# Performance work log

Measured on AMD Instinct MI355X. Metric: run time of the kernel, lower is better.

## Reference

```python
import jax, jax.numpy as jnp
import numpy as np

E = 768   # embedding_dim
D = 64    # head_dim
B = 8
S = 2048


def setup_inputs() -> dict:
    key = jax.random.key(0)
    k1, k2, k3, k4 = jax.random.split(key, 4)
    inputs = jax.random.normal(k1, (B, S, E), dtype=jnp.float32)
    # causal mask: 1 where attending allowed, 0 elsewhere (masked_fill where ==0)
    attention_mask = jnp.tril(jnp.ones((S, S), dtype=jnp.int32))[None, :, :]
    Q = jax.random.normal(k2, (E, D), dtype=jnp.float32) * 0.01
    K = jax.random.normal(k3, (E, D), dtype=jnp.float32) * 0.01
    V = jax.random.normal(k4, (E, D), dtype=jnp.float32) * 0.01
    return {"inputs": inputs, "attention_mask": attention_mask, "Q": Q, "K": K, "V": V}


def reference(inputs, attention_mask, Q, K, V):
    scale = 1.0 / np.sqrt(D).astype(np.float32)
    q = inputs @ Q          # [B,S,D]
    k = inputs @ K          # [B,S,D]
    v = inputs @ V          # [B,S,D]
    w = jnp.einsum('bqd,bkd->bqk', q, k) * scale   # [B,S,S]
    w = jnp.where(attention_mask == 0, -jnp.inf, w)
    attn = jax.nn.softmax(w, axis=-1)              # [B,S,S]
    states = attn @ v                              # [B,S,D] (dropout p=0.0 is identity)
    return states
```

## Files before the change

### kernel.cpp

```cpp
#include <hip/hip_runtime.h>
#include <cstdint>

#define B_ 8
#define S_ 2048
#define E_ 768
#define D_ 64
#define NSPLIT 4
#define SEGLEN (S_ / NSPLIT)
#define ROWS (B_ * S_)

typedef unsigned short ushort_t;
typedef __attribute__((ext_vector_type(8))) short s16x8;
typedef __attribute__((ext_vector_type(4))) float f32x4;

__device__ inline ushort_t f2bf(float f) {
  unsigned int x = __float_as_uint(f);
  return (ushort_t)((x + 0x7fffu + ((x >> 16) & 1u)) >> 16);
}

__device__ inline unsigned int pkbf(float hi, float lo) {
  return __builtin_amdgcn_perm(__float_as_uint(hi) + 0x8000u,
                               __float_as_uint(lo) + 0x8000u, 0x07060302u);
}

__device__ inline void async16(const void* g, void* l) {
  __builtin_amdgcn_global_load_lds(
      (const __attribute__((address_space(1))) unsigned int*)g,
      (__attribute__((address_space(3))) unsigned int*)l, 16, 0, 0);
}

__global__ __launch_bounds__(256) void wt_kernel(
    const float* __restrict__ Wq, const float* __restrict__ Wk,
    const float* __restrict__ Wv, ushort_t* __restrict__ wt) {
  const int mat = blockIdx.y;
  const int e = blockIdx.x * 4 + (threadIdx.x >> 6);
  const int d = threadIdx.x & 63;
  const float* W = (mat == 0) ? Wq : ((mat == 1) ? Wk : Wv);
  wt[(long)(mat * 64 + d) * E_ + e] = f2bf(W[(long)e * D_ + d]);
}

__global__ __launch_bounds__(256) void qkv_mfma(
    const float* __restrict__ in, const ushort_t* __restrict__ wt,
    ushort_t* __restrict__ qb, ushort_t* __restrict__ kb,
    ushort_t* __restrict__ vtb) {
  const int tid = threadIdx.x;
  const int w = tid >> 6;
  const int L = tid & 63;
  const int c = L & 15;
  const int q = L >> 4;
  const int row0 = blockIdx.x * 32;

  __shared__ float Alds[2][32][64];
  __shared__ ushort_t Blds[2][192][64];

  const int ar0 = w * 8 + (L >> 4);
  const int ar1 = ar0 + 4;
  const int asl = L & 15;
  const float* asrc0 = in + (long)(row0 + ar0) * E_ + ((asl ^ (ar0 & 15)) << 2);
  const float* asrc1 = in + (long)(row0 + ar1) * E_ + ((asl ^ (ar1 & 15)) << 2);
  const int bsl = L & 7;
  const ushort_t* bsrc[6];
#pragma unroll
  for (int jj = 0; jj < 6; ++jj) {
    const int br = w * 48 + jj * 8 + (L >> 3);
    bsrc[jj] = wt + (long)br * E_ + ((bsl ^ (br & 7)) << 3);
  }
  float* ad[2] = {&Alds[0][w * 8][0], &Alds[1][w * 8][0]};
  ushort_t* bd[2] = {&Blds[0][w * 48][0], &Blds[1][w * 48][0]};

  const int mloc = w & 1;
  const int nbase = (w >> 1) * 6;
  const int ra = mloc * 16 + c;
  const int offA00 = ra * 256 + ((2 * q + 0) ^ c) * 16;
  const int offA01 = ra * 256 + ((2 * q + 1) ^ c) * 16;
  const int offA10 = ra * 256 + ((8 + 2 * q + 0) ^ c) * 16;
  const int offA11 = ra * 256 + ((8 + 2 * q + 1) ^ c) * 16;
  int offB0[6], offB1[6];
#pragma unroll
  for (int t = 0; t < 6; ++t) {
    const int n = (nbase + t) * 16 + c;
    offB0[t] = n * 128 + ((q + 0) ^ (c & 7)) * 16;
    offB1[t] = n * 128 + ((q + 4) ^ (c & 7)) * 16;
  }
  const char* Abase = (const char*)&Alds[0][0][0];
  const char* Bbase = (const char*)&Blds[0][0][0];

  f32x4 acc[6];
#pragma unroll
  for (int n = 0; n < 6; ++n) acc[n] = (f32x4){0.f, 0.f, 0.f, 0.f};

  async16(asrc0, ad[0]);
  async16(asrc1, ad[0] + 4 * 64);
#pragma unroll
  for (int jj = 0; jj < 6; ++jj) async16(bsrc[jj], bd[0] + jj * 8 * 64);
  asrc0 += 64; asrc1 += 64;
#pragma unroll
  for (int jj = 0; jj < 6; ++jj) bsrc[jj] += 64;

  for (int it = 0; it < E_ / 64; ++it) {
    const int b = it & 1;
    __syncthreads();
    if (it + 1 < E_ / 64) {
      const int nb = 1 - b;
      async16(asrc0, ad[nb]);
      async16(asrc1, ad[nb] + 4 * 64);
#pragma unroll
      for (int jj = 0; jj < 6; ++jj) async16(bsrc[jj], bd[nb] + jj * 8 * 64);
      asrc0 += 64; asrc1 += 64;
#pragma unroll
      for (int jj = 0; jj < 6; ++jj) bsrc[jj] += 64;
    }
    const char* Ab = Abase + b * 8192;
    const char* Bb = Bbase + b * 24576;
    const float4 a00 = *(const float4*)(Ab + offA00);
    const float4 a01 = *(const float4*)(Ab + offA01);
    const float4 a10 = *(const float4*)(Ab + offA10);
    const float4 a11 = *(const float4*)(Ab + offA11);
    union { s16x8 v; unsigned int u[4]; } af0, af1;
    af0.u[0] = pkbf(a00.y, a00.x);
    af0.u[1] = pkbf(a00.w, a00.z);
    af0.u[2] = pkbf(a01.y, a01.x);
    af0.u[3] = pkbf(a01.w, a01.z);
    af1.u[0] = pkbf(a10.y, a10.x);
    af1.u[1] = pkbf(a10.w, a10.z);
    af1.u[2] = pkbf(a11.y, a11.x);
    af1.u[3] = pkbf(a11.w, a11.z);
#pragma unroll
    for (int t = 0; t < 6; ++t) {
      const s16x8 bf0 = *(const s16x8*)(Bb + offB0[t]);
      const s16x8 bf1 = *(const s16x8*)(Bb + offB1[t]);
      acc[t] = __builtin_amdgcn_mfma_f32_16x16x32_bf16(af0.v, bf0, acc[t], 0, 0, 0);
      acc[t] = __builtin_amdgcn_mfma_f32_16x16x32_bf16(af1.v, bf1, acc[t], 0, 0, 0);
    }
  }

  const float qscale = 0.125f * 1.44269504088896340736f;
  const int row0w = row0 + mloc * 16;
  const int b_ = row0w >> 11;
  const int srow = row0w & (S_ - 1);
#pragma unroll
  for (int n = 0; n < 6; ++n) {
    const int gn = nbase + n;
    const int mat = gn >> 2;
    const int d0 = (gn & 3) * 16 + c;
#pragma unroll
    for (int reg = 0; reg < 4; ++reg) {
      const int m = q * 4 + reg;
      const float x = acc[n][reg];
      if (mat == 0) {
        qb[(long)(row0w + m) * D_ + d0] = f2bf(x * qscale);
      } else if (mat == 1) {
        kb[(long)(row0w + m) * D_ + d0] = f2bf(x);
      } else {
        vtb[(long)b_ * D_ * S_ + (long)d0 * S_ + srow + m] = f2bf(x);
      }
    }
  }
}

__global__ __launch_bounds__(256) void attn_mfma(
    const ushort_t* __restrict__ qb, const ushort_t* __restrict__ kb,
    const ushort_t* __restrict__ vtb, float* __restrict__ op,
    float* __restrict__ lw) {
  const int qb0 = blockIdx.x * 64;
  const int batch = blockIdx.y;
  const int seg = blockIdx.z;
  const int j0 = seg * SEGLEN;
  const int jmax = min(j0 + SEGLEN, qb0 + 64);
  if (j0 >= jmax) return;
  const int ntiles = (jmax - j0) >> 6;

  const int w = threadIdx.x >> 6;
  const int L = threadIdx.x & 63;
  const int col = L & 15;
  const int quad = L >> 4;

  __shared__ ushort_t Kl[2][64][64];
  __shared__ ushort_t Vl[2][64][64];
  __shared__ ushort_t Pl[4][16][72];

  const ushort_t* kbb = kb + (long)batch * S_ * D_;
  const ushort_t* vbb = vtb + (long)batch * D_ * S_;

  const int rl = (w << 4) + (L >> 3);
  const int gsw = (L & 7) ^ (rl & 7);
  const ushort_t* ksrc = kbb + ((long)(j0 + rl) << 6) + gsw * 8;
  const ushort_t* vsrc = vbb + (long)rl * S_ + j0 + gsw * 8;
  ushort_t* kdst[2] = {&Kl[0][w * 16][0], &Kl[1][w * 16][0]};
  ushort_t* vdst[2] = {&Vl[0][w * 16][0], &Vl[1][w * 16][0]};

  const int s0 = ((quad ^ (col & 7)) * 16);

  const ushort_t* qrow = qb + ((long)(batch * S_ + qb0 + w * 16 + col) * D_);
  const s16x8 qf0 = *(const s16x8*)(qrow + quad * 8);
  const s16x8 qf1 = *(const s16x8*)(qrow + 32 + quad * 8);

  f32x4 O[4];
#pragma unroll
  for (int t = 0; t < 4; ++t) O[t] = (f32x4){0.f, 0.f, 0.f, 0.f};
  float l[4] = {0.f, 0.f, 0.f, 0.f};

  async16(ksrc, kdst[0]);
  async16(ksrc + 512, kdst[0] + 512);
  async16(vsrc, vdst[0]);
  async16(vsrc + 8 * S_, vdst[0] + 512);
  ksrc += 64 * 64; vsrc += 64;

  for (int i = 0; i < ntiles; ++i) {
    const int b = i & 1;
    const int kt = j0 + i * 64;
    __syncthreads();
    if (i + 1 < ntiles) {
      const int nb = 1 - b;
      async16(ksrc, kdst[nb]);
      async16(ksrc + 512, kdst[nb] + 512);
      async16(vsrc, vdst[nb]);
      async16(vsrc + 8 * S_, vdst[nb] + 512);
      ksrc += 64 * 64; vsrc += 64;
    }
    const char* Kb = (const char*)&Kl[b][0][0];
    const char* Vb = (const char*)&Vl[b][0][0];

    f32x4 S[4];
#pragma unroll
    for (int t = 0; t < 4; ++t) {
      const s16x8 kf0 = *(const s16x8*)(Kb + (t * 16 + col) * 128 + s0);
      const s16x8 kf1 = *(const s16x8*)(Kb + (t * 16 + col) * 128 + (s0 ^ 64));
      f32x4 z = (f32x4){0.f, 0.f, 0.f, 0.f};
      z = __builtin_amdgcn_mfma_f32_16x16x32_bf16(qf0, kf0, z, 0, 0, 0);
      S[t] = __builtin_amdgcn_mfma_f32_16x16x32_bf16(qf1, kf1, z, 0, 0, 0);
    }
    if (kt + 64 > qb0) {
#pragma unroll
      for (int t = 0; t < 4; ++t) {
        const int colg = kt + t * 16 + col;
#pragma unroll
        for (int reg = 0; reg < 4; ++reg) {
          const int rowg = qb0 + w * 16 + quad * 4 + reg;
          if (colg > rowg) S[t][reg] = -1e30f;
        }
      }
    }
    float P[4][4];
#pragma unroll
    for (int t = 0; t < 4; ++t)
#pragma unroll
      for (int reg = 0; reg < 4; ++reg) {
        P[t][reg] = exp2f(S[t][reg]);
        l[reg] += P[t][reg];
      }
#pragma unroll
    for (int t = 0; t < 4; ++t)
#pragma unroll
      for (int reg = 0; reg < 4; ++reg)
        Pl[w][quad * 4 + reg][t * 16 + col] = f2bf(P[t][reg]);
    const s16x8 p0 = *(const s16x8*)&Pl[w][col][quad * 8];
    const s16x8 p1 = *(const s16x8*)&Pl[w][col][32 + quad * 8];
#pragma unroll
    for (int t = 0; t < 4; ++t) {
      const s16x8 vf0 = *(const s16x8*)(Vb + (t * 16 + col) * 128 + s0);
      const s16x8 vf1 = *(const s16x8*)(Vb + (t * 16 + col) * 128 + (s0 ^ 64));
      O[t] = __builtin_amdgcn_mfma_f32_16x16x32_bf16(p0, vf0, O[t], 0, 0, 0);
      O[t] = __builtin_amdgcn_mfma_f32_16x16x32_bf16(p1, vf1, O[t], 0, 0, 0);
    }
  }
#pragma unroll
  for (int off = 1; off < 16; off <<= 1)
#pragma unroll
    for (int reg = 0; reg < 4; ++reg)
      l[reg] += __shfl_xor(l[reg], off);

  const int growbase = batch * S_ + qb0 + w * 16;
#pragma unroll
  for (int t = 0; t < 4; ++t)
#pragma unroll
    for (int reg = 0; reg < 4; ++reg)
      op[((long)seg * ROWS + growbase + quad * 4 + reg) * D_ + t * 16 + col] =
          O[t][reg];
  if (col == 0) {
#pragma unroll
    for (int reg = 0; reg < 4; ++reg)
      lw[(long)seg * ROWS + growbase + quad * 4 + reg] = l[reg];
  }
}

__global__ __launch_bounds__(256) void attn_combine(
    const float* __restrict__ op, const float* __restrict__ lw,
    float* __restrict__ out) {
  const int t = threadIdx.x;
  const int d = t & 63;
  const int g = blockIdx.x * 4 + (t >> 6);
  const int s_q = g & (S_ - 1);
  float osum = 0.f, lsum = 0.f;
#pragma unroll
  for (int s = 0; s < NSPLIT; ++s) {
    if (s_q >= s * SEGLEN) {
      osum += op[((long)s * ROWS + g) * D_ + d];
      lsum += lw[(long)s * ROWS + g];
    }
  }
  out[(long)g * D_ + d] = osum / lsum;
}

extern "C" void kernel_launch(void* const* d_in, const int* in_sizes, int n_in,
                              void* d_out, int out_size, void* d_ws, size_t ws_size,
                              hipStream_t stream) {
  const float* in = (const float*)d_in[0];
  const float* Wq = (const float*)d_in[2];
  const float* Wk = (const float*)d_in[3];
  const float* Wv = (const float*)d_in[4];
  float* out = (float*)d_out;

  ushort_t* qbuf = (ushort_t*)d_ws;
  ushort_t* kbuf = qbuf + (long)ROWS * D_;
  ushort_t* vtb = kbuf + (long)ROWS * D_;
  float* op = (float*)(vtb + (long)ROWS * D_);
  float* lw = op + (long)NSPLIT * ROWS * D_;
  ushort_t* wt = (ushort_t*)(lw + (long)NSPLIT * ROWS);

  wt_kernel<<<dim3(E_ / 4, 3), 256, 0, stream>>>(Wq, Wk, Wv, wt);
  qkv_mfma<<<ROWS / 32, 256, 0, stream>>>(in, wt, qbuf, kbuf, vtb);
  attn_mfma<<<dim3(S_ / 64, B_, NSPLIT), 256, 0, stream>>>(qbuf, kbuf, vtb, op, lw);
  attn_combine<<<(ROWS * D_) / 256, 256, 0, stream>>>(op, lw, out);
}
```

Before: 140.3 us.

## Give each wave an independent 16-row attention task and read K/V directly from global memory

The attention kernel is reorganised so every wave owns its own 16-query-row, one-segment task. A flat 640-block grid enumerates only the causally non-empty (batch, segment, query-tile) combinations, so no blocks exit early. The shared-memory double-buffered async K/V staging and the block barriers are removed, and each wave loads K and V fragments straight from global memory into registers. This is meant to cut idle blocks and barrier stalls and to give finer load balance. The cost is roughly four times more K/V reads from L2 and load latency that is no longer hidden by prefetching.

```diff
diff --git a/kernel.cpp b/kernel.cpp
--- a/kernel.cpp
+++ b/kernel.cpp
@@ -162,36 +162,30 @@
     const ushort_t* __restrict__ qb, const ushort_t* __restrict__ kb,
     const ushort_t* __restrict__ vtb, float* __restrict__ op,
     float* __restrict__ lw) {
-  const int qb0 = blockIdx.x * 64;
-  const int batch = blockIdx.y;
-  const int seg = blockIdx.z;
-  const int j0 = seg * SEGLEN;
-  const int jmax = min(j0 + SEGLEN, qb0 + 64);
-  if (j0 >= jmax) return;
-  const int ntiles = (jmax - j0) >> 6;
-
   const int w = threadIdx.x >> 6;
   const int L = threadIdx.x & 63;
   const int col = L & 15;
   const int quad = L >> 4;
 
-  __shared__ ushort_t Kl[2][64][64];
-  __shared__ ushort_t Vl[2][64][64];
+  const int task = blockIdx.x * 4 + w;
+  const int batch = task / 320;
+  const int r = task % 320;
+  int seg, qtl;
+  if (r < 128)      { seg = 0; qtl = r; }
+  else if (r < 224) { seg = 1; qtl = r - 96; }
+  else if (r < 288) { seg = 2; qtl = r - 160; }
+  else              { seg = 3; qtl = r - 192; }
+
+  const int j0 = seg * SEGLEN;
+  const int q0 = qtl * 16;
+  const int jmax = min(j0 + SEGLEN, q0 + 16);
+  const int ntiles = (jmax - j0 + 63) >> 6;
+
   __shared__ ushort_t Pl[4][16][72];
 
   const ushort_t* kbb = kb + (long)batch * S_ * D_;
   const ushort_t* vbb = vtb + (long)batch * D_ * S_;
-
-  const int rl = (w << 4) + (L >> 3);
-  const int gsw = (L & 7) ^ (rl & 7);
-  const ushort_t* ksrc = kbb + ((long)(j0 + rl) << 6) + gsw * 8;
-  const ushort_t* vsrc = vbb + (long)rl * S_ + j0 + gsw * 8;
-  ushort_t* kdst[2] = {&Kl[0][w * 16][0], &Kl[1][w * 16][0]};
-  ushort_t* vdst[2] = {&Vl[0][w * 16][0], &Vl[1][w * 16][0]};
-
-  const int s0 = ((quad ^ (col & 7)) * 16);
-
-  const ushort_t* qrow = qb + ((long)(batch * S_ + qb0 + w * 16 + col) * D_);
+  const ushort_t* qrow = qb + (long)(batch * S_ + q0 + col) * D_;
   const s16x8 qf0 = *(const s16x8*)(qrow + quad * 8);
   const s16x8 qf1 = *(const s16x8*)(qrow + 32 + quad * 8);
 
@@ -200,44 +194,36 @@
   for (int t = 0; t < 4; ++t) O[t] = (f32x4){0.f, 0.f, 0.f, 0.f};
   float l[4] = {0.f, 0.f, 0.f, 0.f};
 
-  async16(ksrc, kdst[0]);
-  async16(ksrc + 512, kdst[0] + 512);
-  async16(vsrc, vdst[0]);
-  async16(vsrc + 8 * S_, vdst[0] + 512);
-  ksrc += 64 * 64; vsrc += 64;
-
   for (int i = 0; i < ntiles; ++i) {
-    const int b = i & 1;
     const int kt = j0 + i * 64;
-    __syncthreads();
-    if (i + 1 < ntiles) {
-      const int nb = 1 - b;
-      async16(ksrc, kdst[nb]);
-      async16(ksrc + 512, kdst[nb] + 512);
-      async16(vsrc, vdst[nb]);
-      async16(vsrc + 8 * S_, vdst[nb] + 512);
-      ksrc += 64 * 64; vsrc += 64;
-    }
-    const char* Kb = (const char*)&Kl[b][0][0];
-    const char* Vb = (const char*)&Vl[b][0][0];
-
-    f32x4 S[4];
+    s16x8 kf0[4], kf1[4], vf0[4], vf1[4];
 #pragma unroll
     for (int t = 0; t < 4; ++t) {
-      const s16x8 kf0 = *(const s16x8*)(Kb + (t * 16 + col) * 128 + s0);
-      const s16x8 kf1 = *(const s16x8*)(Kb + (t * 16 + col) * 128 + (s0 ^ 64));
+      const ushort_t* kr = kbb + ((long)(kt + t * 16 + col) << 6) + quad * 8;
+      kf0[t] = *(const s16x8*)kr;
+      kf1[t] = *(const s16x8*)(kr + 32);
+    }
+#pragma unroll
+    for (int t = 0; t < 4; ++t) {
+      const ushort_t* vr = vbb + (long)(t * 16 + col) * S_ + kt + quad * 8;
+      vf0[t] = *(const s16x8*)vr;
+      vf1[t] = *(const s16x8*)(vr + 32);
+    }
+    f32x4 Sv[4];
+#pragma unroll
+    for (int t = 0; t < 4; ++t) {
       f32x4 z = (f32x4){0.f, 0.f, 0.f, 0.f};
-      z = __builtin_amdgcn_mfma_f32_16x16x32_bf16(qf0, kf0, z, 0, 0, 0);
-      S[t] = __builtin_amdgcn_mfma_f32_16x16x32_bf16(qf1, kf1, z, 0, 0, 0);
-    }
-    if (kt + 64 > qb0) {
+      z = __builtin_amdgcn_mfma_f32_16x16x32_bf16(qf0, kf0[t], z, 0, 0, 0);
+      Sv[t] = __builtin_amdgcn_mfma_f32_16x16x32_bf16(qf1, kf1[t], z, 0, 0, 0);
+    }
+    if (kt + 63 > q0) {
 #pragma unroll
       for (int t = 0; t < 4; ++t) {
         const int colg = kt + t * 16 + col;
 #pragma unroll
         for (int reg = 0; reg < 4; ++reg) {
-          const int rowg = qb0 + w * 16 + quad * 4 + reg;
-          if (colg > rowg) S[t][reg] = -1e30f;
+          const int rowg = q0 + quad * 4 + reg;
+          if (colg > rowg) Sv[t][reg] = -1e30f;
         }
       }
     }
@@ -246,7 +232,7 @@
     for (int t = 0; t < 4; ++t)
 #pragma unroll
       for (int reg = 0; reg < 4; ++reg) {
-        P[t][reg] = exp2f(S[t][reg]);
+        P[t][reg] = exp2f(Sv[t][reg]);
         l[reg] += P[t][reg];
       }
 #pragma unroll
@@ -258,10 +244,8 @@
     const s16x8 p1 = *(const s16x8*)&Pl[w][col][32 + quad * 8];
 #pragma unroll
     for (int t = 0; t < 4; ++t) {
-      const s16x8 vf0 = *(const s16x8*)(Vb + (t * 16 + col) * 128 + s0);
-      const s16x8 vf1 = *(const s16x8*)(Vb + (t * 16 + col) * 128 + (s0 ^ 64));
-      O[t] = __builtin_amdgcn_mfma_f32_16x16x32_bf16(p0, vf0, O[t], 0, 0, 0);
-      O[t] = __builtin_amdgcn_mfma_f32_16x16x32_bf16(p1, vf1, O[t], 0, 0, 0);
+      O[t] = __builtin_amdgcn_mfma_f32_16x16x32_bf16(p0, vf0[t], O[t], 0, 0, 0);
+      O[t] = __builtin_amdgcn_mfma_f32_16x16x32_bf16(p1, vf1[t], O[t], 0, 0, 0);
     }
   }
 #pragma unroll
@@ -270,7 +254,7 @@
     for (int reg = 0; reg < 4; ++reg)
       l[reg] += __shfl_xor(l[reg], off);
 
-  const int growbase = batch * S_ + qb0 + w * 16;
+  const int growbase = batch * S_ + q0;
 #pragma unroll
   for (int t = 0; t < 4; ++t)
 #pragma unroll
@@ -320,6 +304,6 @@
 
   wt_kernel<<<dim3(E_ / 4, 3), 256, 0, stream>>>(Wq, Wk, Wv, wt);
   qkv_mfma<<<ROWS / 32, 256, 0, stream>>>(in, wt, qbuf, kbuf, vtb);
-  attn_mfma<<<dim3(S_ / 64, B_, NSPLIT), 256, 0, stream>>>(qbuf, kbuf, vtb, op, lw);
+  attn_mfma<<<640, 256, 0, stream>>>(qbuf, kbuf, vtb, op, lw);
   attn_combine<<<(ROWS * D_) / 256, 256, 0, stream>>>(op, lw, out);
 }
```

New measurement: 162.8 us. 16.0% more time.
